# Kernel optimization log

Measured on AMD Instinct MI355X. Metric: run time of the kernel, lower is better.

## Reference

```python
import jax, jax.numpy as jnp
import numpy as np


def setup_inputs() -> dict:
    key = jax.random.key(0)
    k1, k2 = jax.random.split(key)
    B, C, N = 8, 3, 4096
    X = jax.random.normal(k1, (B, C, N), dtype=jnp.float32)
    Y = jax.random.normal(k2, (B, C, N), dtype=jnp.float32)
    return {"X": X, "Y": Y, "ps": N}


def reference(X, Y, ps):
    # X, Y: [B, C, N] -> permute to [B, N, C] point clouds
    A = jnp.transpose(X, (0, 2, 1))  # [B, N, C]
    Bp = jnp.transpose(Y, (0, 2, 1))  # [B, ps, C]
    r = jnp.sum(A * A, axis=2)[:, :, None]      # [B, N, 1]
    r1 = jnp.sum(Bp * Bp, axis=2)[:, None, :]   # [B, 1, ps]
    # squared pairwise distances: ||a||^2 - 2 a.b + ||b||^2 -> [B, N, ps]
    t = r - 2.0 * jnp.einsum('bnc,bmc->bnm', A, Bp) + r1
    d1 = jnp.min(t, axis=1)  # min over A points: [B, ps]
    d2 = jnp.min(t, axis=2)  # min over B points: [B, N]
    ls = (d1 + d2) / 2.0     # requires N == ps (as in original repeat logic)
    return jnp.mean(ls)
```

## Files before the change

### kernel.cpp

```cpp
#include <hip/hip_runtime.h>


typedef __attribute__((ext_vector_type(8))) short short8;
typedef __attribute__((ext_vector_type(16))) float f32x16;
typedef __attribute__((ext_vector_type(4))) unsigned uint4v;

constexpr int NPTS  = 4096;
constexpr int NB    = 8;
constexpr int NQ    = 2 * NB * NPTS;
constexpr int TSN   = 4;
constexpr int TGT   = 1024;
constexpr int TILES = TGT / 32;
constexpr int GRID_MAIN  = 16 * 8 * TSN;
constexpr int RED_BLOCKS = 64;

__device__ inline unsigned short f2bf(float x) {
    unsigned u = __float_as_uint(x);
    unsigned r = u + 0x7fff + ((u >> 16) & 1);
    return (unsigned short)(r >> 16);
}
__device__ inline float bf2f(unsigned short h) {
    return __uint_as_float(((unsigned)h) << 16);
}
__device__ inline unsigned pack2(unsigned short a, unsigned short b) {
    return (unsigned)a | ((unsigned)b << 16);
}

__global__ __launch_bounds__(256, 2) void chamfer_main(
    const float* __restrict__ X, const float* __restrict__ Y,
    float* __restrict__ minq)
{
    __shared__ char BL[TGT * 32];

    const int bid  = blockIdx.x;
    const int ts   = bid & 3;
    const int qg   = (bid >> 2) & 7;
    const int pair = bid >> 5;
    const int dir  = pair >> 3, b = pair & 7;
    const int tid  = threadIdx.x;
    const int lane = tid & 63, wv = tid >> 6;
    const int c    = lane & 31, h = lane >> 5;

    const float* __restrict__ Qraw = (dir ? Y : X) + b * 3 * NPTS;
    const float* __restrict__ Traw = (dir ? X : Y) + b * 3 * NPTS;

    #pragma unroll
    for (int k = 0; k < 4; ++k) {
        const int p = k * 256 + tid;
        const int i = ts * TGT + p;
        float tx = Traw[i], ty = Traw[NPTS + i], tz = Traw[2 * NPTS + i];
        float r  = fmaf(tx, tx, fmaf(ty, ty, tz * tz));
        unsigned short hx = f2bf(tx), lx = f2bf(tx - bf2f(hx));
        unsigned short hy = f2bf(ty), ly = f2bf(ty - bf2f(hy));
        unsigned short hz = f2bf(tz), lz = f2bf(tz - bf2f(hz));
        unsigned short hr = f2bf(r),  lr = f2bf(r  - bf2f(hr));
        unsigned w0 = pack2(hx, lx), w2 = pack2(hy, ly), w4 = pack2(hz, lz);
        unsigned w6 = pack2(hr, lr);
        uint4v lo = {w0, w0, w2, w2};
        uint4v hi = {w4, w4, w6, 0u};
        const int sw = (p >> 2) & 1;
        *(uint4v*)(BL + p * 32 + ((0 ^ sw) << 4)) = lo;
        *(uint4v*)(BL + p * 32 + ((1 ^ sw) << 4)) = hi;
    }

    union Frag { uint4v u; short8 s; };
    Frag qfr[4];
    float ra[4];
    #pragma unroll
    for (int s = 0; s < 4; ++s) {
        const int q = qg * 512 + wv * 128 + s * 32 + c;
        float qx = Qraw[q], qy = Qraw[NPTS + q], qz = Qraw[2 * NPTS + q];
        ra[s] = fmaf(qx, qx, fmaf(qy, qy, qz * qz));
        float mx = -2.f * qx, my = -2.f * qy, mz = -2.f * qz;
        unsigned short hx = f2bf(mx), lx = f2bf(mx - bf2f(hx));
        unsigned short hy = f2bf(my), ly = f2bf(my - bf2f(hy));
        unsigned short hz = f2bf(mz), lz = f2bf(mz - bf2f(hz));
        uint4v f0 = {pack2(hx, hx), pack2(lx, lx), pack2(hy, hy), pack2(ly, ly)};
        uint4v f1 = {pack2(hz, hz), pack2(lz, lz), 0x3F803F80u, 0u};
        Frag f; f.u = h ? f1 : f0;
        qfr[s] = f;
    }

    __syncthreads();

    f32x16 run[4];
    #pragma unroll
    for (int s = 0; s < 4; ++s)
        #pragma unroll
        for (int i = 0; i < 16; ++i) run[s][i] = 3.4e38f;
    f32x16 zacc;
    #pragma unroll
    for (int i = 0; i < 16; ++i) zacc[i] = 0.f;

    const char* base = BL + c * 32 + ((h ^ ((c >> 2) & 1)) << 4);

    short8 tf0 = *(const short8*)(base);
    short8 tf1 = *(const short8*)(base + 1024);
    for (int t = 0; t < TILES; t += 2) {
        const int t2 = (t + 2) & (TILES - 1);
        const int t3 = (t + 3) & (TILES - 1);
        short8 nf0 = *(const short8*)(base + t2 * 1024);
        short8 nf1 = *(const short8*)(base + t3 * 1024);
        #pragma unroll
        for (int s = 0; s < 4; ++s) {
            f32x16 dA = __builtin_amdgcn_mfma_f32_32x32x16_bf16(tf0, qfr[s].s, zacc, 0, 0, 0);
            f32x16 dB = __builtin_amdgcn_mfma_f32_32x32x16_bf16(tf1, qfr[s].s, zacc, 0, 0, 0);
            #pragma unroll
            for (int i = 0; i < 16; ++i)
                run[s][i] = fminf(run[s][i], fminf(dA[i], dB[i]));
        }
        tf0 = nf0; tf1 = nf1;
    }

    #pragma unroll
    for (int s = 0; s < 4; ++s) {
        float m0 = fminf(fminf(run[s][0],  run[s][1]),  fminf(run[s][2],  run[s][3]));
        float m1 = fminf(fminf(run[s][4],  run[s][5]),  fminf(run[s][6],  run[s][7]));
        float m2 = fminf(fminf(run[s][8],  run[s][9]),  fminf(run[s][10], run[s][11]));
        float m3 = fminf(fminf(run[s][12], run[s][13]), fminf(run[s][14], run[s][15]));
        float m  = fminf(fminf(m0, m1), fminf(m2, m3));
        m = fminf(m, __shfl_xor(m, 32));
        m += ra[s];
        if (h == 0)
            minq[(size_t)ts * NQ + pair * 4096 + qg * 512 + wv * 128 + s * 32 + c] = m;
    }
}

__global__ __launch_bounds__(256) void chamfer_reduce(
    const float4* __restrict__ mq4, float* __restrict__ partials,
    unsigned* __restrict__ counter, float* __restrict__ out)
{
    __shared__ float wsum[4];
    __shared__ int   fireFlag;
    const int tid = threadIdx.x;
    const int lane = tid & 63, wv = tid >> 6;
    const int idx = blockIdx.x * 256 + tid;

    float4 m = mq4[idx];
    #pragma unroll
    for (int s = 1; s < TSN; ++s) {
        float4 v = mq4[(size_t)s * (NQ / 4) + idx];
        m.x = fminf(m.x, v.x); m.y = fminf(m.y, v.y);
        m.z = fminf(m.z, v.z); m.w = fminf(m.w, v.w);
    }
    float v = (m.x + m.y) + (m.z + m.w);
    #pragma unroll
    for (int off = 1; off < 64; off <<= 1) v += __shfl_xor(v, off);
    if (lane == 0) wsum[wv] = v;
    __syncthreads();
    if (tid == 0) {
        partials[blockIdx.x] = (wsum[0] + wsum[1]) + (wsum[2] + wsum[3]);
        __threadfence();
        unsigned old = atomicAdd(counter, 1u);
        fireFlag = ((old & 63u) == 63u);
    }
    __syncthreads();

    if (fireFlag) {
        __threadfence();
        if (tid < 64) {
            float p = partials[tid];
            #pragma unroll
            for (int off = 1; off < 64; off <<= 1) p += __shfl_xor(p, off);
            if (tid == 0)
                out[0] = p * (1.0f / 65536.0f);
        }
    }
}

extern "C" void kernel_launch(void* const* d_in, const int* in_sizes, int n_in,
                              void* d_out, int out_size, void* d_ws, size_t ws_size,
                              hipStream_t stream) {
    const float* X = (const float*)d_in[0];
    const float* Y = (const float*)d_in[1];

    float*    minq     = (float*)d_ws;
    float*    partials = minq + (size_t)TSN * NQ;
    unsigned* counter  = (unsigned*)(partials + RED_BLOCKS);
    float*    out      = (float*)d_out;

    chamfer_main<<<GRID_MAIN, 256, 0, stream>>>(X, Y, minq);
    chamfer_reduce<<<RED_BLOCKS, 256, 0, stream>>>(
        (const float4*)minq, partials, counter, out);
}
```

Measured before the change: 20.00 us.

## Split chamfer work into smaller per-wave query tiles with more blocks

Reduces each wave's work from four 32-query fragments to one and halves the target tile per block, growing the grid from 512 to 4096 blocks with 8 target slices. This is meant to raise occupancy and spread work across more CUs, with a higher min-blocks launch bound. In exchange, the target bf16 conversion is repeated by many more blocks, each LDS fragment feeds one MFMA instead of four, the register prefetch is dropped, and twice as many partial minima are written for the reduction.

```diff
diff --git a/kernel.cpp b/kernel.cpp
--- a/kernel.cpp
+++ b/kernel.cpp
@@ -8,10 +8,10 @@
 constexpr int NPTS  = 4096;
 constexpr int NB    = 8;
 constexpr int NQ    = 2 * NB * NPTS;
-constexpr int TSN   = 4;
-constexpr int TGT   = 1024;
+constexpr int TSN   = 8;
+constexpr int TGT   = 512;
 constexpr int TILES = TGT / 32;
-constexpr int GRID_MAIN  = 16 * 8 * TSN;
+constexpr int GRID_MAIN  = 16 * 32 * TSN;
 constexpr int RED_BLOCKS = 64;
 
 __device__ inline unsigned short f2bf(float x) {
@@ -26,16 +26,16 @@
     return (unsigned)a | ((unsigned)b << 16);
 }
 
-__global__ __launch_bounds__(256, 2) void chamfer_main(
+__global__ __launch_bounds__(256, 8) void chamfer_main(
     const float* __restrict__ X, const float* __restrict__ Y,
     float* __restrict__ minq)
 {
     __shared__ char BL[TGT * 32];
 
     const int bid  = blockIdx.x;
-    const int ts   = bid & 3;
-    const int qg   = (bid >> 2) & 7;
-    const int pair = bid >> 5;
+    const int ts   = bid & 7;
+    const int qg   = (bid >> 3) & 31;
+    const int pair = bid >> 8;
     const int dir  = pair >> 3, b = pair & 7;
     const int tid  = threadIdx.x;
     const int lane = tid & 63, wv = tid >> 6;
@@ -45,7 +45,7 @@
     const float* __restrict__ Traw = (dir ? X : Y) + b * 3 * NPTS;
 
     #pragma unroll
-    for (int k = 0; k < 4; ++k) {
+    for (int k = 0; k < 2; ++k) {
         const int p = k * 256 + tid;
         const int i = ts * TGT + p;
         float tx = Traw[i], ty = Traw[NPTS + i], tz = Traw[2 * NPTS + i];
@@ -64,65 +64,50 @@
     }
 
     union Frag { uint4v u; short8 s; };
-    Frag qfr[4];
-    float ra[4];
-    #pragma unroll
-    for (int s = 0; s < 4; ++s) {
-        const int q = qg * 512 + wv * 128 + s * 32 + c;
+    Frag qfr;
+    float ra;
+    {
+        const int q = qg * 128 + wv * 32 + c;
         float qx = Qraw[q], qy = Qraw[NPTS + q], qz = Qraw[2 * NPTS + q];
-        ra[s] = fmaf(qx, qx, fmaf(qy, qy, qz * qz));
+        ra = fmaf(qx, qx, fmaf(qy, qy, qz * qz));
         float mx = -2.f * qx, my = -2.f * qy, mz = -2.f * qz;
         unsigned short hx = f2bf(mx), lx = f2bf(mx - bf2f(hx));
         unsigned short hy = f2bf(my), ly = f2bf(my - bf2f(hy));
         unsigned short hz = f2bf(mz), lz = f2bf(mz - bf2f(hz));
         uint4v f0 = {pack2(hx, hx), pack2(lx, lx), pack2(hy, hy), pack2(ly, ly)};
         uint4v f1 = {pack2(hz, hz), pack2(lz, lz), 0x3F803F80u, 0u};
-        Frag f; f.u = h ? f1 : f0;
-        qfr[s] = f;
+        qfr.u = h ? f1 : f0;
     }
 
     __syncthreads();
 
-    f32x16 run[4];
+    f32x16 run;
     #pragma unroll
-    for (int s = 0; s < 4; ++s)
-        #pragma unroll
-        for (int i = 0; i < 16; ++i) run[s][i] = 3.4e38f;
+    for (int i = 0; i < 16; ++i) run[i] = 3.4e38f;
     f32x16 zacc;
     #pragma unroll
     for (int i = 0; i < 16; ++i) zacc[i] = 0.f;
 
     const char* base = BL + c * 32 + ((h ^ ((c >> 2) & 1)) << 4);
 
-    short8 tf0 = *(const short8*)(base);
-    short8 tf1 = *(const short8*)(base + 1024);
-    for (int t = 0; t < TILES; t += 2) {
-        const int t2 = (t + 2) & (TILES - 1);
-        const int t3 = (t + 3) & (TILES - 1);
-        short8 nf0 = *(const short8*)(base + t2 * 1024);
-        short8 nf1 = *(const short8*)(base + t3 * 1024);
+    for (int t = 0; t < TILES; ++t) {
+        short8 tf = *(const short8*)(base + t * 1024);
+        f32x16 dA = __builtin_amdgcn_mfma_f32_32x32x16_bf16(tf, qfr.s, zacc, 0, 0, 0);
         #pragma unroll
-        for (int s = 0; s < 4; ++s) {
-            f32x16 dA = __builtin_amdgcn_mfma_f32_32x32x16_bf16(tf0, qfr[s].s, zacc, 0, 0, 0);
-            f32x16 dB = __builtin_amdgcn_mfma_f32_32x32x16_bf16(tf1, qfr[s].s, zacc, 0, 0, 0);
-            #pragma unroll
-            for (int i = 0; i < 16; ++i)
-                run[s][i] = fminf(run[s][i], fminf(dA[i], dB[i]));
-        }
-        tf0 = nf0; tf1 = nf1;
+        for (int i = 0; i < 16; ++i)
+            run[i] = fminf(run[i], dA[i]);
     }
 
-    #pragma unroll
-    for (int s = 0; s < 4; ++s) {
-        float m0 = fminf(fminf(run[s][0],  run[s][1]),  fminf(run[s][2],  run[s][3]));
-        float m1 = fminf(fminf(run[s][4],  run[s][5]),  fminf(run[s][6],  run[s][7]));
-        float m2 = fminf(fminf(run[s][8],  run[s][9]),  fminf(run[s][10], run[s][11]));
-        float m3 = fminf(fminf(run[s][12], run[s][13]), fminf(run[s][14], run[s][15]));
+    {
+        float m0 = fminf(fminf(run[0],  run[1]),  fminf(run[2],  run[3]));
+        float m1 = fminf(fminf(run[4],  run[5]),  fminf(run[6],  run[7]));
+        float m2 = fminf(fminf(run[8],  run[9]),  fminf(run[10], run[11]));
+        float m3 = fminf(fminf(run[12], run[13]), fminf(run[14], run[15]));
         float m  = fminf(fminf(m0, m1), fminf(m2, m3));
         m = fminf(m, __shfl_xor(m, 32));
-        m += ra[s];
+        m += ra;
         if (h == 0)
-            minq[(size_t)ts * NQ + pair * 4096 + qg * 512 + wv * 128 + s * 32 + c] = m;
+            minq[(size_t)ts * NQ + pair * 4096 + qg * 128 + wv * 32 + c] = m;
     }
 }
 
```

Result: slower. 24.22 us (+21.1%).

## Precompute bf16-split target image in prep kernel and DMA it into LDS

Applied to the files above, without the earlier changes.

Adds a prep kernel that converts each point cloud into the swizzled hi/lo bf16 LDS image once. The main kernel then copies that image straight into shared memory with global_load_lds instead of each block redoing the conversion for its tile. This removes conversion work repeated across query groups, at the cost of an extra kernel launch and a global round trip of the image. The prep kernel also resets the reduction counter.

```diff
diff --git a/kernel.cpp b/kernel.cpp
--- a/kernel.cpp
+++ b/kernel.cpp
@@ -13,6 +13,7 @@
 constexpr int TILES = TGT / 32;
 constexpr int GRID_MAIN  = 16 * 8 * TSN;
 constexpr int RED_BLOCKS = 64;
+constexpr size_t IMG_BYTES = (size_t)NPTS * 32;
 
 __device__ inline unsigned short f2bf(float x) {
     unsigned u = __float_as_uint(x);
@@ -26,7 +27,38 @@
     return (unsigned)a | ((unsigned)b << 16);
 }
 
+__global__ __launch_bounds__(256) void chamfer_prep(
+    const float* __restrict__ X, const float* __restrict__ Y,
+    char* __restrict__ Timg, unsigned* __restrict__ counter)
+{
+    const int P     = blockIdx.x * 256 + threadIdx.x;
+    const int cloud = P >> 15;
+    const int b     = (P >> 12) & 7;
+    const int p     = P & 4095;
+
+    if (P == 0) *counter = 0;
+
+    const float* src = (cloud ? Y : X) + b * 3 * NPTS + p;
+    const float tx = src[0], ty = src[NPTS], tz = src[2 * NPTS];
+    const float r  = fmaf(tx, tx, fmaf(ty, ty, tz * tz));
+
+    unsigned short hx = f2bf(tx), lx = f2bf(tx - bf2f(hx));
+    unsigned short hy = f2bf(ty), ly = f2bf(ty - bf2f(hy));
+    unsigned short hz = f2bf(tz), lz = f2bf(tz - bf2f(hz));
+    unsigned short hr = f2bf(r),  lr = f2bf(r  - bf2f(hr));
+    unsigned w0 = pack2(hx, lx), w2 = pack2(hy, ly), w4 = pack2(hz, lz);
+    unsigned w6 = pack2(hr, lr);
+    uint4v lo = {w0, w0, w2, w2};
+    uint4v hi = {w4, w4, w6, 0u};
+
+    char* tb = Timg + (size_t)(cloud * NB + b) * IMG_BYTES + (size_t)p * 32;
+    const int sw = (p >> 2) & 1;
+    *(uint4v*)(tb + ((0 ^ sw) << 4)) = lo;
+    *(uint4v*)(tb + ((1 ^ sw) << 4)) = hi;
+}
+
 __global__ __launch_bounds__(256, 2) void chamfer_main(
+    const char* __restrict__ Timg,
     const float* __restrict__ X, const float* __restrict__ Y,
     float* __restrict__ minq)
 {
@@ -42,25 +74,18 @@
     const int c    = lane & 31, h = lane >> 5;
 
     const float* __restrict__ Qraw = (dir ? Y : X) + b * 3 * NPTS;
-    const float* __restrict__ Traw = (dir ? X : Y) + b * 3 * NPTS;
-
-    #pragma unroll
-    for (int k = 0; k < 4; ++k) {
-        const int p = k * 256 + tid;
-        const int i = ts * TGT + p;
-        float tx = Traw[i], ty = Traw[NPTS + i], tz = Traw[2 * NPTS + i];
-        float r  = fmaf(tx, tx, fmaf(ty, ty, tz * tz));
-        unsigned short hx = f2bf(tx), lx = f2bf(tx - bf2f(hx));
-        unsigned short hy = f2bf(ty), ly = f2bf(ty - bf2f(hy));
-        unsigned short hz = f2bf(tz), lz = f2bf(tz - bf2f(hz));
-        unsigned short hr = f2bf(r),  lr = f2bf(r  - bf2f(hr));
-        unsigned w0 = pack2(hx, lx), w2 = pack2(hy, ly), w4 = pack2(hz, lz);
-        unsigned w6 = pack2(hr, lr);
-        uint4v lo = {w0, w0, w2, w2};
-        uint4v hi = {w4, w4, w6, 0u};
-        const int sw = (p >> 2) & 1;
-        *(uint4v*)(BL + p * 32 + ((0 ^ sw) << 4)) = lo;
-        *(uint4v*)(BL + p * 32 + ((1 ^ sw) << 4)) = hi;
+
+    {
+        const char* gsrc = Timg + (size_t)((1 - dir) * NB + b) * IMG_BYTES
+                         + (size_t)ts * (TGT * 32) + tid * 16;
+        char* ldst = BL + tid * 16;
+        #pragma unroll
+        for (int j = 0; j < 8; ++j) {
+            __builtin_amdgcn_global_load_lds(
+                (const __attribute__((address_space(1))) void*)(gsrc + j * 4096),
+                (__attribute__((address_space(3))) void*)(ldst + j * 4096),
+                16, 0, 0);
+        }
     }
 
     union Frag { uint4v u; short8 s; };
@@ -174,12 +199,14 @@
     const float* X = (const float*)d_in[0];
     const float* Y = (const float*)d_in[1];
 
-    float*    minq     = (float*)d_ws;
+    char*     Timg     = (char*)d_ws;
+    float*    minq     = (float*)(Timg + 16 * IMG_BYTES);
     float*    partials = minq + (size_t)TSN * NQ;
     unsigned* counter  = (unsigned*)(partials + RED_BLOCKS);
     float*    out      = (float*)d_out;
 
-    chamfer_main<<<GRID_MAIN, 256, 0, stream>>>(X, Y, minq);
+    chamfer_prep<<<256, 256, 0, stream>>>(X, Y, Timg, counter);
+    chamfer_main<<<GRID_MAIN, 256, 0, stream>>>(Timg, X, Y, minq);
     chamfer_reduce<<<RED_BLOCKS, 256, 0, stream>>>(
         (const float4*)minq, partials, counter, out);
 }
```

Result: slower. 25.80 us (+29.0%).
